# Optimization experiments

Measured on AMD Instinct MI355X. Metric: run time of the kernel, lower is better.

## Reference

```python
import jax, jax.numpy as jnp
import numpy as np

B, T, D, H = 2, 2048, 1024, 16


def setup_inputs() -> dict:
    key = jax.random.key(0)
    kx, kq, kk, kv, ko = jax.random.split(key, 5)
    s = D ** -0.5  # linear-layer init scale
    return {
        "x": jax.random.normal(kx, (B, T, D), dtype=jnp.float32),
        "Wq": jax.random.normal(kq, (D, D), dtype=jnp.float32) * s,
        "Wk": jax.random.normal(kk, (D, D), dtype=jnp.float32) * s,
        "Wv": jax.random.normal(kv, (D, D), dtype=jnp.float32) * s,
        "Wo": jax.random.normal(ko, (D, D), dtype=jnp.float32) * s,
        "quadrant_weights": jnp.array([1.0, -0.5, -0.5, 0.25], dtype=jnp.float32),
    }


def reference(x, Wq, Wk, Wv, Wo, quadrant_weights):
    Bx, Tx, Dx = x.shape
    d = Dx // H          # head dim
    h = d // 2           # quadrant (half-head) dim
    scale = h ** -0.5

    # projections -> (B, H, T, d)
    q = (x @ Wq).reshape(Bx, Tx, H, d).transpose(0, 2, 1, 3)
    k = (x @ Wk).reshape(Bx, Tx, H, d).transpose(0, 2, 1, 3)
    v = (x @ Wv).reshape(Bx, Tx, H, d).transpose(0, 2, 1, 3)

    q1, q2 = q[..., :h], q[..., h:]
    k1, k2 = k[..., :h], k[..., h:]

    w = jax.nn.softmax(quadrant_weights)
    # Fused quadrant sum: w0*q1k1^T + w1*q1k2^T + w2*q2k1^T + w3*q2k2^T
    # == q1 @ (w0*k1 + w1*k2)^T + q2 @ (w2*k1 + w3*k2)^T  (same math, fewer matmuls)
    k_eff1 = w[0] * k1 + w[1] * k2
    k_eff2 = w[2] * k1 + w[3] * k2
    attn = (jnp.einsum('bhqc,bhkc->bhqk', q1, k_eff1)
            + jnp.einsum('bhqc,bhkc->bhqk', q2, k_eff2)) * scale
    attn = jax.nn.softmax(attn, axis=-1)

    out = jnp.einsum('bhqk,bhkd->bhqd', attn, v)
    out = out.transpose(0, 2, 1, 3).reshape(Bx, Tx, Dx)
    return out @ Wo
```

## Files before the change

kernel.cpp:

```cpp
#include <hip/hip_runtime.h>

typedef unsigned short u16;
typedef unsigned int u32;
typedef __attribute__((ext_vector_type(8))) short short8;
typedef __attribute__((ext_vector_type(4))) short short4v;
typedef __attribute__((ext_vector_type(4))) float f32x4;
typedef __attribute__((ext_vector_type(16))) float f32x16;
typedef __attribute__((ext_vector_type(2))) unsigned u32x2;
typedef __attribute__((ext_vector_type(4))) unsigned u32x4;

__device__ __forceinline__ u16 f2bf(float f) {
  union { float f; unsigned u; } a; a.f = f;
  unsigned u = a.u + 0x7fffu + ((a.u >> 16) & 1u);
  return (u16)(u >> 16);
}
__device__ __forceinline__ u32 cvtpk(float lo, float hi_) {
  u32 r; asm("v_cvt_pk_bf16_f32 %0, %1, %2" : "=v"(r) : "v"(lo), "v"(hi_)); return r;
}
__device__ __forceinline__ void plswap(u32 &x, u32 &y) {
  asm("v_permlane32_swap_b32 %0, %1" : "+v"(x), "+v"(y));
}
__device__ __forceinline__ short8 as_short8(u32x4 v) {
  union { u32x4 u; short8 s; } c; c.u = v; return c.s;
}
__device__ __forceinline__ float max3f(float a, float b, float c) {
  return fmaxf(fmaxf(a, b), c);
}
__device__ __forceinline__ void gload16(const u16* g, u16* l) {
  __builtin_amdgcn_global_load_lds(
      (__attribute__((address_space(1))) void*)(u16*)g,
      (__attribute__((address_space(3))) void*)l, 16, 0, 0);
}
__device__ __forceinline__ void keep8(short8 v) {
  union { short8 s; int i[4]; } u; u.s = v;
  asm volatile("" :: "v"(u.i[0]), "v"(u.i[1]), "v"(u.i[2]), "v"(u.i[3]));
}
__device__ __forceinline__ void wait_vm4() { asm volatile("s_waitcnt vmcnt(4)" ::: "memory"); }
__device__ __forceinline__ void wait_vm3() { asm volatile("s_waitcnt vmcnt(3)" ::: "memory"); }
__device__ __forceinline__ void wait_vm0() { asm volatile("s_waitcnt vmcnt(0)" ::: "memory"); }
__device__ __forceinline__ void barrier_raw() {
  __builtin_amdgcn_sched_barrier(0);
  __builtin_amdgcn_s_barrier();
  __builtin_amdgcn_sched_barrier(0);
}

__global__ void cvt_x_kernel(const float* __restrict__ x, u16* __restrict__ xb) {
  int i = (blockIdx.x * 256 + threadIdx.x) * 8;
  float4 a = *(const float4*)(x + i);
  float4 b = *(const float4*)(x + i + 4);
  short8 v;
  v[0] = (short)f2bf(a.x); v[1] = (short)f2bf(a.y);
  v[2] = (short)f2bf(a.z); v[3] = (short)f2bf(a.w);
  v[4] = (short)f2bf(b.x); v[5] = (short)f2bf(b.y);
  v[6] = (short)f2bf(b.z); v[7] = (short)f2bf(b.w);
  *(short8*)(xb + i) = v;
}

__global__ void prep_w_kernel(const float* __restrict__ Wq, const float* __restrict__ Wk,
                              const float* __restrict__ Wv, const float* __restrict__ Wo,
                              const float* __restrict__ qw,
                              u16* __restrict__ Wcat, u16* __restrict__ Wot) {
  __shared__ float tile[32][33];
  const int z = blockIdx.z;
  const int n0 = blockIdx.x * 32, k0 = blockIdx.y * 32;
  const float* src = (z == 0) ? Wq : (z == 1) ? Wk : (z == 2) ? Wv : Wo;
  float w0 = 0.f, w1 = 0.f, w2 = 0.f, w3 = 0.f;
  if (z == 1) {
    float a = qw[0], b = qw[1], c = qw[2], d = qw[3];
    float mx = fmaxf(fmaxf(a, b), fmaxf(c, d));
    float ea = expf(a - mx), eb = expf(b - mx), ec = expf(c - mx), ed = expf(d - mx);
    float s = ea + eb + ec + ed;
    w0 = ea / s; w1 = eb / s; w2 = ec / s; w3 = ed / s;
  }
  #pragma unroll
  for (int i = 0; i < 32; i += 8) {
    int k = k0 + threadIdx.y + i;
    int n = n0 + threadIdx.x;
    float v;
    if (z == 1) {
      int c = n & 63;
      if (c < 32) v = w0 * src[k * 1024 + n]      + w1 * src[k * 1024 + n + 32];
      else        v = w2 * src[k * 1024 + n - 32] + w3 * src[k * 1024 + n];
    } else {
      v = src[k * 1024 + n];
    }
    tile[threadIdx.y + i][threadIdx.x] = v;
  }
  __syncthreads();
  #pragma unroll
  for (int i = 0; i < 32; i += 8) {
    int n = n0 + threadIdx.y + i;
    int k = k0 + threadIdx.x;
    u16 v = f2bf(tile[threadIdx.x][threadIdx.y + i]);
    if (z < 3) Wcat[(size_t)(z * 1024 + n) * 1024 + k] = v;
    else       Wot[(size_t)n * 1024 + k] = v;
  }
}

template<int MODE, int BM>
__global__ __launch_bounds__(256, 2)
void gemm_k(const u16* __restrict__ A, const u16* __restrict__ Bm,
            u16* __restrict__ out_q, u16* __restrict__ out_k,
            u16* __restrict__ out_vt, float* __restrict__ out_f) {
  constexpr int WM = BM / 2;
  constexpr int MR = WM / 16;
  __shared__ u16 At[3][BM * 32];
  __shared__ u16 Bt[3][128 * 32];
  const int tid = threadIdx.x;
  const int wid = tid >> 6, lane = tid & 63;
  const int l15 = lane & 15, l4 = lane >> 4;

  const int nwg = gridDim.x * gridDim.y;
  const int cpx = nwg >> 3;
  int bid = blockIdx.y * gridDim.x + blockIdx.x;
  int wg = (bid & 7) * cpx + (bid >> 3);
  const int bx = wg % gridDim.x, by = wg / gridDim.x;
  const int mblk = by * BM, nblk = bx * 128;
  const int wm = (wid >> 1) * WM, wn = (wid & 1) * 64;
  f32x4 acc[MR][4] = {};

  const int rr = lane >> 2;
  const int cA = (lane & 3) * 8;
  const u16* gB = Bm + (size_t)(nblk + wid * 32 + rr) * 1024 + cA;
  const u16* gA = (BM == 128) ? A + (size_t)(mblk + wid * 32 + rr) * 1024 + cA
                              : A + (size_t)(mblk + wid * 16 + rr) * 1024 + cA;

  auto STAGE = [&](int ib, int kt) {
    if constexpr (BM == 128) {
      #pragma unroll
      for (int q = 0; q < 2; ++q)
        gload16(gA + (size_t)q * 16 * 1024 + kt, &At[ib][(wid * 32 + q * 16) * 32]);
    } else {
      gload16(gA + kt, &At[ib][(wid * 16) * 32]);
    }
    #pragma unroll
    for (int q = 0; q < 2; ++q)
      gload16(gB + (size_t)q * 16 * 1024 + kt, &Bt[ib][(wid * 32 + q * 16) * 32]);
  };

  STAGE(0, 0);
  STAGE(1, 32);
  int ib = 0, ibw = 2;
  for (int s = 0; s < 32; ++s) {
    if (s < 31) { if constexpr (BM == 128) wait_vm4(); else wait_vm3(); }
    else wait_vm0();
    barrier_raw();
    if (s + 2 < 32) STAGE(ibw, (s + 2) * 32);
    short8 af[MR], bf[4];
    #pragma unroll
    for (int i = 0; i < MR; ++i)
      af[i] = *(const short8*)(&At[ib][(wm + i * 16 + l15) * 32 + l4 * 8]);
    #pragma unroll
    for (int j = 0; j < 4; ++j)
      bf[j] = *(const short8*)(&Bt[ib][(wn + j * 16 + l15) * 32 + l4 * 8]);
    #pragma unroll
    for (int i = 0; i < MR; ++i)
      #pragma unroll
      for (int j = 0; j < 4; ++j)
        acc[i][j] = __builtin_amdgcn_mfma_f32_16x16x32_bf16(af[i], bf[j], acc[i][j], 0, 0, 0);
    ib = (ib == 2) ? 0 : ib + 1;
    ibw = (ibw == 2) ? 0 : ibw + 1;
  }

  const float QSCALE = 0.17677669529663687f * 1.4426950408889634f;
  #pragma unroll
  for (int i = 0; i < MR; ++i) {
    int m_g = mblk + wm + i * 16 + l4 * 4;
    #pragma unroll
    for (int j = 0; j < 4; ++j) {
      int n_g = nblk + wn + j * 16 + l15;
      f32x4 v = acc[i][j];
      if (MODE == 1) {
        #pragma unroll
        for (int jj = 0; jj < 4; ++jj)
          out_f[(size_t)(m_g + jj) * 1024 + n_g] = v[jj];
      } else {
        if (n_g < 2048) {
          u16* dst; float sc;
          if (n_g < 1024) { dst = out_q; sc = QSCALE; } else { dst = out_k; sc = 1.0f; }
          int nn = n_g & 1023;
          #pragma unroll
          for (int jj = 0; jj < 4; ++jj)
            dst[(size_t)(m_g + jj) * 1024 + nn] = f2bf(v[jj] * sc);
        } else {
          int c = n_g - 2048;
          int b = m_g >> 11, t = m_g & 2047;
          short4v p;
          p[0] = (short)f2bf(v[0]); p[1] = (short)f2bf(v[1]);
          p[2] = (short)f2bf(v[2]); p[3] = (short)f2bf(v[3]);
          *(short4v*)(out_vt + ((size_t)((b << 4) + (c >> 6)) * 64 + (c & 63)) * 2048 + t) = p;
        }
      }
    }
  }
}

__global__ __launch_bounds__(256)
void attn_k(const u16* __restrict__ Q, const u16* __restrict__ Kb,
            const u16* __restrict__ Vt, u16* __restrict__ O) {
  __shared__ u16 lk[3][64 * 64];
  __shared__ u16 lv[3][64 * 64];
  const int tid = threadIdx.x, wid = tid >> 6, lane = tid & 63;
  const int l31 = lane & 31, hi = lane >> 5;

  int bid = blockIdx.y * 16 + blockIdx.x;
  int wg = (bid & 7) * 64 + (bid >> 3);
  const int qt = wg & 15, bh = wg >> 4;
  const int b = bh >> 4, h = bh & 15;
  const int qrow = qt * 128 + wid * 32 + l31;

  short8 qf[4];
  #pragma unroll
  for (int cs = 0; cs < 4; ++cs)
    qf[cs] = *(const short8*)(Q + (size_t)(b * 2048 + qrow) * 1024 + h * 64 + cs * 16 + hi * 8);
  #pragma unroll
  for (int cs = 0; cs < 4; ++cs) keep8(qf[cs]);

  const int sr = lane >> 3;
  const int sc8 = (lane & 7) ^ sr;
  const u16* Kg = Kb + (size_t)b * 2048 * 1024 + h * 64 + sc8 * 8;
  const u16* Vg = Vt + (size_t)bh * 64 * 2048 + sc8 * 8;
  const int s0i = wid * 2;
  const int swz = l31 & 7;

  short8 onesf;
  #pragma unroll
  for (int j = 0; j < 8; ++j) onesf[j] = (short)0x3F80;
  const f32x16 z16 = {};

  f32x16 accO0 = {}, accO1 = {}, sacc = {};
  float mrun = -1e30f;

  auto STAGE = [&](int tt, int ibx) {
    #pragma unroll
    for (int s2 = 0; s2 < 2; ++s2) {
      int s = s0i + s2;
      int r = s * 8 + sr;
      gload16(Kg + (size_t)(tt * 64 + r) * 1024, &lk[ibx][s * 512]);
      gload16(Vg + (size_t)r * 2048 + tt * 64, &lv[ibx][s * 512]);
    }
  };

  STAGE(0, 0);
  STAGE(1, 1);
  int ib = 0, ibw = 2;

  for (int t = 0; t < 32; ++t) {
    if (t < 31) wait_vm4(); else wait_vm0();
    barrier_raw();
    if (t + 2 < 32) STAGE(t + 2, ibw);

    const u16* kb = lk[ib];
    const u16* vb = lv[ib];

    f32x16 s0v, s1v;
    __builtin_amdgcn_s_setprio(1);
    {
      short8 k0 = *(const short8*)(kb + l31 * 64 + (((0 * 2 + hi) ^ swz) * 8));
      short8 k1 = *(const short8*)(kb + (32 + l31) * 64 + (((0 * 2 + hi) ^ swz) * 8));
      s0v = __builtin_amdgcn_mfma_f32_32x32x16_bf16(k0, qf[0], z16, 0, 0, 0);
      s1v = __builtin_amdgcn_mfma_f32_32x32x16_bf16(k1, qf[0], z16, 0, 0, 0);
    }
    #pragma unroll
    for (int cs = 1; cs < 4; ++cs) {
      int ch = cs * 2 + hi;
      short8 k0 = *(const short8*)(kb + l31 * 64 + ((ch ^ swz) * 8));
      short8 k1 = *(const short8*)(kb + (32 + l31) * 64 + ((ch ^ swz) * 8));
      s0v = __builtin_amdgcn_mfma_f32_32x32x16_bf16(k0, qf[cs], s0v, 0, 0, 0);
      s1v = __builtin_amdgcn_mfma_f32_32x32x16_bf16(k1, qf[cs], s1v, 0, 0, 0);
    }
    __builtin_amdgcn_s_setprio(0);

    float m01 = max3f(s0v[0], s0v[1], s0v[2]);
    float m02 = max3f(s0v[3], s0v[4], s0v[5]);
    float m03 = max3f(s0v[6], s0v[7], s0v[8]);
    float m04 = max3f(s0v[9], s0v[10], s0v[11]);
    float m05 = max3f(s0v[12], s0v[13], s0v[14]);
    float m11 = max3f(s1v[0], s1v[1], s1v[2]);
    float m12 = max3f(s1v[3], s1v[4], s1v[5]);
    float m13 = max3f(s1v[6], s1v[7], s1v[8]);
    float m14 = max3f(s1v[9], s1v[10], s1v[11]);
    float m15 = max3f(s1v[12], s1v[13], s1v[14]);
    float ma = max3f(m01, m02, m03);
    float mb = max3f(m04, m05, s0v[15]);
    float mc = max3f(m11, m12, m13);
    float md = max3f(m14, m15, s1v[15]);
    float mx = fmaxf(fmaxf(ma, mb), fmaxf(mc, md));
    mx = fmaxf(mx, __shfl_xor(mx, 32, 64));

    if (!__all(mx <= mrun + 8.0f)) {
      float mnew = fmaxf(mrun, mx);
      float al = exp2f(mrun - mnew);
      mrun = mnew;
      sacc[0] *= al;
      #pragma unroll
      for (int i = 0; i < 16; ++i) { accO0[i] *= al; accO1[i] *= al; }
    }

    #pragma unroll
    for (int i = 0; i < 16; ++i) { s0v[i] = exp2f(s0v[i] - mrun); s1v[i] = exp2f(s1v[i] - mrun); }

    short8 paS[4];
    #pragma unroll
    for (int half = 0; half < 2; ++half) {
      #pragma unroll
      for (int kq = 0; kq < 2; ++kq) {
        float p0, p1, p2, p3, p4, p5, p6, p7;
        if (half == 0) {
          p0 = s0v[kq*8+0]; p1 = s0v[kq*8+1]; p2 = s0v[kq*8+2]; p3 = s0v[kq*8+3];
          p4 = s0v[kq*8+4]; p5 = s0v[kq*8+5]; p6 = s0v[kq*8+6]; p7 = s0v[kq*8+7];
        } else {
          p0 = s1v[kq*8+0]; p1 = s1v[kq*8+1]; p2 = s1v[kq*8+2]; p3 = s1v[kq*8+3];
          p4 = s1v[kq*8+4]; p5 = s1v[kq*8+5]; p6 = s1v[kq*8+6]; p7 = s1v[kq*8+7];
        }
        u32 A = cvtpk(p0, p1), B = cvtpk(p2, p3);
        u32 C = cvtpk(p4, p5), D = cvtpk(p6, p7);
        plswap(A, C);
        plswap(B, D);
        u32x4 w; w[0] = A; w[1] = B; w[2] = C; w[3] = D;
        paS[half * 2 + kq] = as_short8(w);
      }
    }

    __builtin_amdgcn_s_setprio(1);
    #pragma unroll
    for (int ks = 0; ks < 4; ++ks) {
      int ch = ks * 2 + hi;
      short8 v0 = *(const short8*)(vb + l31 * 64 + ((ch ^ swz) * 8));
      short8 v1 = *(const short8*)(vb + (32 + l31) * 64 + ((ch ^ swz) * 8));
      accO0 = __builtin_amdgcn_mfma_f32_32x32x16_bf16(v0, paS[ks], accO0, 0, 0, 0);
      accO1 = __builtin_amdgcn_mfma_f32_32x32x16_bf16(v1, paS[ks], accO1, 0, 0, 0);
      sacc  = __builtin_amdgcn_mfma_f32_32x32x16_bf16(onesf, paS[ks], sacc, 0, 0, 0);
    }
    __builtin_amdgcn_s_setprio(0);

    ib = (ib == 2) ? 0 : ib + 1;
    ibw = (ibw == 2) ? 0 : ibw + 1;
  }

  float inv = 1.0f / sacc[0];
  u16* Op = O + (size_t)(b * 2048 + qrow) * 1024 + h * 64;
  #pragma unroll
  for (int g = 0; g < 4; ++g) {
    u32x2 pr;
    pr[0] = cvtpk(accO0[4*g] * inv, accO0[4*g+1] * inv);
    pr[1] = cvtpk(accO0[4*g+2] * inv, accO0[4*g+3] * inv);
    *(u32x2*)(Op + 8*g + 4*hi) = pr;
    u32x2 pr2;
    pr2[0] = cvtpk(accO1[4*g] * inv, accO1[4*g+1] * inv);
    pr2[1] = cvtpk(accO1[4*g+2] * inv, accO1[4*g+3] * inv);
    *(u32x2*)(Op + 32 + 8*g + 4*hi) = pr2;
  }
}

extern "C" void kernel_launch(void* const* d_in, const int* in_sizes, int n_in,
                              void* d_out, int out_size, void* d_ws, size_t ws_size,
                              hipStream_t stream) {
  const float* x  = (const float*)d_in[0];
  const float* Wq = (const float*)d_in[1];
  const float* Wk = (const float*)d_in[2];
  const float* Wv = (const float*)d_in[3];
  const float* Wo = (const float*)d_in[4];
  const float* qw = (const float*)d_in[5];

  char* w = (char*)d_ws;
  u16* xb   = (u16*)(w);
  u16* Wcat = (u16*)(w + (8u  << 20));
  u16* Wot  = (u16*)(w + (14u << 20));
  u16* Qb   = (u16*)(w + (16u << 20));
  u16* Kb   = (u16*)(w + (24u << 20));
  u16* Vtb  = (u16*)(w + (32u << 20));
  u16* Ob   = (u16*)(w + (40u << 20));

  cvt_x_kernel<<<2048, 256, 0, stream>>>(x, xb);
  prep_w_kernel<<<dim3(32, 32, 4), dim3(32, 8), 0, stream>>>(Wq, Wk, Wv, Wo, qw, Wcat, Wot);
  gemm_k<0, 128><<<dim3(24, 32), 256, 0, stream>>>(xb, Wcat, Qb, Kb, Vtb, nullptr);
  attn_k<<<dim3(16, 32), 256, 0, stream>>>(Qb, Kb, Vtb, Ob);
  gemm_k<1, 64><<<dim3(8, 64), 256, 0, stream>>>(Ob, Wot, nullptr, nullptr, nullptr, (float*)d_out);
}
```

Measured before the change: 136.3 us.

## Load K/V fragments directly from global memory instead of LDS staging

Replaces the triple-buffered LDS pipeline (global_load_lds plus barriers) in the attention kernel with direct per-lane global loads of K and V MFMA fragments into registers, unrolled by two. This removes LDS traffic, the swizzle and the block barriers, and each wave then reads K/V independently. It gives up sharing across the four waves, so global/L2 traffic for K/V rises fourfold and load latency is no longer hidden by an explicit prefetch stage.

```diff
diff --git a/kernel.cpp b/kernel.cpp
--- a/kernel.cpp
+++ b/kernel.cpp
@@ -30,10 +30,6 @@
   __builtin_amdgcn_global_load_lds(
       (__attribute__((address_space(1))) void*)(u16*)g,
       (__attribute__((address_space(3))) void*)l, 16, 0, 0);
-}
-__device__ __forceinline__ void keep8(short8 v) {
-  union { short8 s; int i[4]; } u; u.s = v;
-  asm volatile("" :: "v"(u.i[0]), "v"(u.i[1]), "v"(u.i[2]), "v"(u.i[3]));
 }
 __device__ __forceinline__ void wait_vm4() { asm volatile("s_waitcnt vmcnt(4)" ::: "memory"); }
 __device__ __forceinline__ void wait_vm3() { asm volatile("s_waitcnt vmcnt(3)" ::: "memory"); }
@@ -198,8 +194,6 @@
 __global__ __launch_bounds__(256)
 void attn_k(const u16* __restrict__ Q, const u16* __restrict__ Kb,
             const u16* __restrict__ Vt, u16* __restrict__ O) {
-  __shared__ u16 lk[3][64 * 64];
-  __shared__ u16 lv[3][64 * 64];
   const int tid = threadIdx.x, wid = tid >> 6, lane = tid & 63;
   const int l31 = lane & 31, hi = lane >> 5;
 
@@ -213,15 +207,10 @@
   #pragma unroll
   for (int cs = 0; cs < 4; ++cs)
     qf[cs] = *(const short8*)(Q + (size_t)(b * 2048 + qrow) * 1024 + h * 64 + cs * 16 + hi * 8);
-  #pragma unroll
-  for (int cs = 0; cs < 4; ++cs) keep8(qf[cs]);
-
-  const int sr = lane >> 3;
-  const int sc8 = (lane & 7) ^ sr;
-  const u16* Kg = Kb + (size_t)b * 2048 * 1024 + h * 64 + sc8 * 8;
-  const u16* Vg = Vt + (size_t)bh * 64 * 2048 + sc8 * 8;
-  const int s0i = wid * 2;
-  const int swz = l31 & 7;
+
+  const u16* Kp0 = Kb + (size_t)(b * 2048 + l31) * 1024 + h * 64;
+  const u16* Vp0 = Vt + (size_t)(bh * 64 + l31) * 2048;
+  const u16* Vp1 = Vt + (size_t)(bh * 64 + 32 + l31) * 2048;
 
   short8 onesf;
   #pragma unroll
@@ -231,43 +220,28 @@
   f32x16 accO0 = {}, accO1 = {}, sacc = {};
   float mrun = -1e30f;
 
-  auto STAGE = [&](int tt, int ibx) {
-    #pragma unroll
-    for (int s2 = 0; s2 < 2; ++s2) {
-      int s = s0i + s2;
-      int r = s * 8 + sr;
-      gload16(Kg + (size_t)(tt * 64 + r) * 1024, &lk[ibx][s * 512]);
-      gload16(Vg + (size_t)r * 2048 + tt * 64, &lv[ibx][s * 512]);
-    }
-  };
-
-  STAGE(0, 0);
-  STAGE(1, 1);
-  int ib = 0, ibw = 2;
-
+  #pragma unroll 2
   for (int t = 0; t < 32; ++t) {
-    if (t < 31) wait_vm4(); else wait_vm0();
-    barrier_raw();
-    if (t + 2 < 32) STAGE(t + 2, ibw);
-
-    const u16* kb = lk[ib];
-    const u16* vb = lv[ib];
+    const int kt = t * 64;
+
+    short8 kf0[4], kf1[4], vf0[4], vf1[4];
+    #pragma unroll
+    for (int cs = 0; cs < 4; ++cs) {
+      int ch = cs * 2 + hi;
+      kf0[cs] = *(const short8*)(Kp0 + (size_t)kt * 1024 + ch * 8);
+      kf1[cs] = *(const short8*)(Kp0 + (size_t)(kt + 32) * 1024 + ch * 8);
+      vf0[cs] = *(const short8*)(Vp0 + kt + ch * 8);
+      vf1[cs] = *(const short8*)(Vp1 + kt + ch * 8);
+    }
 
     f32x16 s0v, s1v;
     __builtin_amdgcn_s_setprio(1);
-    {
-      short8 k0 = *(const short8*)(kb + l31 * 64 + (((0 * 2 + hi) ^ swz) * 8));
-      short8 k1 = *(const short8*)(kb + (32 + l31) * 64 + (((0 * 2 + hi) ^ swz) * 8));
-      s0v = __builtin_amdgcn_mfma_f32_32x32x16_bf16(k0, qf[0], z16, 0, 0, 0);
-      s1v = __builtin_amdgcn_mfma_f32_32x32x16_bf16(k1, qf[0], z16, 0, 0, 0);
-    }
+    s0v = __builtin_amdgcn_mfma_f32_32x32x16_bf16(kf0[0], qf[0], z16, 0, 0, 0);
+    s1v = __builtin_amdgcn_mfma_f32_32x32x16_bf16(kf1[0], qf[0], z16, 0, 0, 0);
     #pragma unroll
     for (int cs = 1; cs < 4; ++cs) {
-      int ch = cs * 2 + hi;
-      short8 k0 = *(const short8*)(kb + l31 * 64 + ((ch ^ swz) * 8));
-      short8 k1 = *(const short8*)(kb + (32 + l31) * 64 + ((ch ^ swz) * 8));
-      s0v = __builtin_amdgcn_mfma_f32_32x32x16_bf16(k0, qf[cs], s0v, 0, 0, 0);
-      s1v = __builtin_amdgcn_mfma_f32_32x32x16_bf16(k1, qf[cs], s1v, 0, 0, 0);
+      s0v = __builtin_amdgcn_mfma_f32_32x32x16_bf16(kf0[cs], qf[cs], s0v, 0, 0, 0);
+      s1v = __builtin_amdgcn_mfma_f32_32x32x16_bf16(kf1[cs], qf[cs], s1v, 0, 0, 0);
     }
     __builtin_amdgcn_s_setprio(0);
 
@@ -325,17 +299,11 @@
     __builtin_amdgcn_s_setprio(1);
     #pragma unroll
     for (int ks = 0; ks < 4; ++ks) {
-      int ch = ks * 2 + hi;
-      short8 v0 = *(const short8*)(vb + l31 * 64 + ((ch ^ swz) * 8));
-      short8 v1 = *(const short8*)(vb + (32 + l31) * 64 + ((ch ^ swz) * 8));
-      accO0 = __builtin_amdgcn_mfma_f32_32x32x16_bf16(v0, paS[ks], accO0, 0, 0, 0);
-      accO1 = __builtin_amdgcn_mfma_f32_32x32x16_bf16(v1, paS[ks], accO1, 0, 0, 0);
-      sacc  = __builtin_amdgcn_mfma_f32_32x32x16_bf16(onesf, paS[ks], sacc, 0, 0, 0);
+      accO0 = __builtin_amdgcn_mfma_f32_32x32x16_bf16(vf0[ks], paS[ks], accO0, 0, 0, 0);
+      accO1 = __builtin_amdgcn_mfma_f32_32x32x16_bf16(vf1[ks], paS[ks], accO1, 0, 0, 0);
+      sacc  = __builtin_amdgcn_mfma_f32_32x32x16_bf16(onesf,   paS[ks], sacc,  0, 0, 0);
     }
     __builtin_amdgcn_s_setprio(0);
-
-    ib = (ib == 2) ? 0 : ib + 1;
-    ibw = (ibw == 2) ? 0 : ibw + 1;
   }
 
   float inv = 1.0f / sacc[0];
```

After: 187.6 us. 1.38x slower.

## Software-pipeline QK^T one tile ahead with four-deep K/V LDS ring

Applied to the files above, without the earlier changes.

Moves the attention tile loop to a software-pipelined schedule. The QK^T MFMAs for tile t+1 are issued before the softmax and PV work of tile t, and ping-pong score registers are used across a 2x-unrolled loop. The K/V LDS ring grows from three to four buffers so loads can be staged three tiles ahead. This is meant to hide softmax VALU latency behind matrix work and lengthen prefetch distance, at the cost of more VGPRs for the extra score accumulators and more LDS, both of which may reduce occupancy.

```diff
diff --git a/kernel.cpp b/kernel.cpp
--- a/kernel.cpp
+++ b/kernel.cpp
@@ -35,6 +35,7 @@
   union { short8 s; int i[4]; } u; u.s = v;
   asm volatile("" :: "v"(u.i[0]), "v"(u.i[1]), "v"(u.i[2]), "v"(u.i[3]));
 }
+__device__ __forceinline__ void wait_vm8() { asm volatile("s_waitcnt vmcnt(8)" ::: "memory"); }
 __device__ __forceinline__ void wait_vm4() { asm volatile("s_waitcnt vmcnt(4)" ::: "memory"); }
 __device__ __forceinline__ void wait_vm3() { asm volatile("s_waitcnt vmcnt(3)" ::: "memory"); }
 __device__ __forceinline__ void wait_vm0() { asm volatile("s_waitcnt vmcnt(0)" ::: "memory"); }
@@ -198,8 +199,8 @@
 __global__ __launch_bounds__(256)
 void attn_k(const u16* __restrict__ Q, const u16* __restrict__ Kb,
             const u16* __restrict__ Vt, u16* __restrict__ O) {
-  __shared__ u16 lk[3][64 * 64];
-  __shared__ u16 lv[3][64 * 64];
+  __shared__ u16 lk[4][64 * 64];
+  __shared__ u16 lv[4][64 * 64];
   const int tid = threadIdx.x, wid = tid >> 6, lane = tid & 63;
   const int l31 = lane & 31, hi = lane >> 5;
 
@@ -240,36 +241,31 @@
       gload16(Vg + (size_t)r * 2048 + tt * 64, &lv[ibx][s * 512]);
     }
   };
-
-  STAGE(0, 0);
-  STAGE(1, 1);
-  int ib = 0, ibw = 2;
-
-  for (int t = 0; t < 32; ++t) {
-    if (t < 31) wait_vm4(); else wait_vm0();
-    barrier_raw();
-    if (t + 2 < 32) STAGE(t + 2, ibw);
-
-    const u16* kb = lk[ib];
-    const u16* vb = lv[ib];
-
-    f32x16 s0v, s1v;
+  auto QK = [&](int ibx, f32x16& o0, f32x16& o1) {
+    const u16* kb = lk[ibx];
     __builtin_amdgcn_s_setprio(1);
     {
-      short8 k0 = *(const short8*)(kb + l31 * 64 + (((0 * 2 + hi) ^ swz) * 8));
-      short8 k1 = *(const short8*)(kb + (32 + l31) * 64 + (((0 * 2 + hi) ^ swz) * 8));
-      s0v = __builtin_amdgcn_mfma_f32_32x32x16_bf16(k0, qf[0], z16, 0, 0, 0);
-      s1v = __builtin_amdgcn_mfma_f32_32x32x16_bf16(k1, qf[0], z16, 0, 0, 0);
+      short8 k0 = *(const short8*)(kb + l31 * 64 + ((hi ^ swz) * 8));
+      short8 k1 = *(const short8*)(kb + (32 + l31) * 64 + ((hi ^ swz) * 8));
+      o0 = __builtin_amdgcn_mfma_f32_32x32x16_bf16(k0, qf[0], z16, 0, 0, 0);
+      o1 = __builtin_amdgcn_mfma_f32_32x32x16_bf16(k1, qf[0], z16, 0, 0, 0);
     }
     #pragma unroll
     for (int cs = 1; cs < 4; ++cs) {
       int ch = cs * 2 + hi;
       short8 k0 = *(const short8*)(kb + l31 * 64 + ((ch ^ swz) * 8));
       short8 k1 = *(const short8*)(kb + (32 + l31) * 64 + ((ch ^ swz) * 8));
-      s0v = __builtin_amdgcn_mfma_f32_32x32x16_bf16(k0, qf[cs], s0v, 0, 0, 0);
-      s1v = __builtin_amdgcn_mfma_f32_32x32x16_bf16(k1, qf[cs], s1v, 0, 0, 0);
+      o0 = __builtin_amdgcn_mfma_f32_32x32x16_bf16(k0, qf[cs], o0, 0, 0, 0);
+      o1 = __builtin_amdgcn_mfma_f32_32x32x16_bf16(k1, qf[cs], o1, 0, 0, 0);
     }
     __builtin_amdgcn_s_setprio(0);
+  };
+
+  auto BODY = [&](int t, f32x16& s0v, f32x16& s1v, f32x16& n0v, f32x16& n1v) {
+    if (t < 30) wait_vm4(); else wait_vm0();
+    barrier_raw();
+    if (t + 3 < 32) STAGE(t + 3, (t + 3) & 3);
+    if (t + 1 < 32) QK((t + 1) & 3, n0v, n1v);
 
     float m01 = max3f(s0v[0], s0v[1], s0v[2]);
     float m02 = max3f(s0v[3], s0v[4], s0v[5]);
@@ -322,6 +318,7 @@
       }
     }
 
+    const u16* vb = lv[t & 3];
     __builtin_amdgcn_s_setprio(1);
     #pragma unroll
     for (int ks = 0; ks < 4; ++ks) {
@@ -333,9 +330,19 @@
       sacc  = __builtin_amdgcn_mfma_f32_32x32x16_bf16(onesf, paS[ks], sacc, 0, 0, 0);
     }
     __builtin_amdgcn_s_setprio(0);
-
-    ib = (ib == 2) ? 0 : ib + 1;
-    ibw = (ibw == 2) ? 0 : ibw + 1;
+  };
+
+  STAGE(0, 0);
+  STAGE(1, 1);
+  STAGE(2, 2);
+  wait_vm8();
+  barrier_raw();
+  f32x16 sA0, sA1, sB0, sB1;
+  QK(0, sA0, sA1);
+
+  for (int t = 0; t < 32; t += 2) {
+    BODY(t, sA0, sA1, sB0, sB1);
+    BODY(t + 1, sB0, sB1, sA0, sA1);
   }
 
   float inv = 1.0f / sacc[0];
```

Measured after the change: 144.1 us. 1.06x slower.
